# Kernel optimization log

Hardware: AMD Instinct MI355X
Metric: run time of the kernel (lower is better)

The kernel has to match this reference:

```python
import jax, jax.numpy as jnp
import numpy as np

N = 32768; D = 384; P = 3; CORR_D = 2 * 49 * P * P  # 882
G_KK = 4096; G_JK = 512
EPS = 1e-3  # LayerNorm eps in the torch module

FLOAT_NAMES = ("net","inp","corr","corr_w1","corr_b1","corr_w2","corr_b2","corr_ln_g","corr_ln_b","corr_w3","corr_b3","norm_g","norm_b","c1_w1","c1_b1","c1_w2","c1_b2","c2_w1","c2_b1","c2_w2","c2_b2","kk_fw","kk_fb","kk_gw","kk_gb","kk_hw","kk_hb","ij_fw","ij_fb","ij_gw","ij_gb","ij_hw","ij_hb","g_ln1_g","g_ln1_b","g1_gw","g1_gb","g1_r1w","g1_r1b","g1_r2w","g1_r2b","g_ln2_g","g_ln2_b","g2_gw","g2_gb","g2_r1w","g2_r1b","g2_r2w","g2_r2b","d_w","d_b","w_w","w_b")

def _ln(x, g, b):
    m = jnp.mean(x, -1, keepdims=True)
    v = jnp.mean((x - m) ** 2, -1, keepdims=True)
    return (x - m) * jax.lax.rsqrt(v + EPS) * g + b

def _mlp2(x, w1, b1, w2, b2):
    return jax.nn.relu(x @ w1 + b1) @ w2 + b2

def _gated_residual(x, gw, gb, r1w, r1b, r2w, r2b):
    gate = jax.nn.sigmoid(x @ gw + gb)
    res = jax.nn.relu(x @ r1w + r1b) @ r2w + r2b
    return x + gate * res

def _soft_agg(x, jx, fw, fb, gw, gb, hw, hb, num_groups):
    # x: [N, D]; jx: [N] group ids -> group-wise softmax weighted sum
    logits = x @ gw + gb
    feats = x @ fw + fb
    gmax = jax.ops.segment_max(logits, jx, num_segments=num_groups)
    e = jnp.exp(logits - gmax[jx])
    den = jax.ops.segment_sum(e, jx, num_segments=num_groups)
    w = e / (den[jx] + 1e-12)
    y = jax.ops.segment_sum(feats * w, jx, num_segments=num_groups)
    return (y @ hw + hb)[jx]

def _forward(p, nix, njx, ukk, ujk):
    # corr encoder MLP
    h = jax.nn.relu(p["corr"] @ p["corr_w1"] + p["corr_b1"]) @ p["corr_w2"] + p["corr_b2"]
    h = jax.nn.relu(_ln(h, p["corr_ln_g"], p["corr_ln_b"])) @ p["corr_w3"] + p["corr_b3"]
    net = p["net"] + p["inp"] + h
    net = _ln(net, p["norm_g"], p["norm_b"])
    mask_ix = (nix >= 0).astype(net.dtype).reshape(1, -1, 1)
    mask_jx = (njx >= 0).astype(net.dtype).reshape(1, -1, 1)
    net = net + _mlp2(mask_ix * net[:, nix], p["c1_w1"], p["c1_b1"], p["c1_w2"], p["c1_b2"])
    net = net + _mlp2(mask_jx * net[:, njx], p["c2_w1"], p["c2_b1"], p["c2_w2"], p["c2_b2"])
    net = net + _soft_agg(net[0], ukk, p["kk_fw"], p["kk_fb"], p["kk_gw"], p["kk_gb"], p["kk_hw"], p["kk_hb"], G_KK)[None]
    net = net + _soft_agg(net[0], ujk, p["ij_fw"], p["ij_fb"], p["ij_gw"], p["ij_gb"], p["ij_hw"], p["ij_hb"], G_JK)[None]
    net = _ln(net, p["g_ln1_g"], p["g_ln1_b"])
    net = _gated_residual(net, p["g1_gw"], p["g1_gb"], p["g1_r1w"], p["g1_r1b"], p["g1_r2w"], p["g1_r2b"])
    net = _ln(net, p["g_ln2_g"], p["g_ln2_b"])
    net = _gated_residual(net, p["g2_gw"], p["g2_gb"], p["g2_r1w"], p["g2_r1b"], p["g2_r2w"], p["g2_r2b"])
    r = jax.nn.relu(net)
    d = r @ p["d_w"] + p["d_b"]               # GradClip is identity in forward
    w = jax.nn.sigmoid(r @ p["w_w"] + p["w_b"])
    return net, d, w

def setup_inputs() -> dict:
    key = jax.random.key(0)
    it = iter(jax.random.split(key, 64))
    def pr(*shape):
        return jax.random.normal(next(it), shape, dtype=jnp.float32) * 0.02
    z = lambda *s: jnp.zeros(s, jnp.float32)
    o = lambda *s: jnp.ones(s, jnp.float32)
    inp = {
        "net": jax.random.normal(next(it), (1, N, D), dtype=jnp.float32),
        "inp": jax.random.normal(next(it), (1, N, D), dtype=jnp.float32),
        "corr": jax.random.normal(next(it), (1, N, CORR_D), dtype=jnp.float32),
        "nix": jax.random.randint(next(it), (N,), 0, N),
        "njx": jax.random.randint(next(it), (N,), 0, N),
        "ukk": jax.random.randint(next(it), (N,), 0, G_KK),
        "ujk": jax.random.randint(next(it), (N,), 0, G_JK),
        "corr_w1": pr(CORR_D, D), "corr_b1": z(D), "corr_w2": pr(D, D), "corr_b2": z(D),
        "corr_ln_g": o(D), "corr_ln_b": z(D), "corr_w3": pr(D, D), "corr_b3": z(D),
        "norm_g": o(D), "norm_b": z(D),
        "c1_w1": pr(D, D), "c1_b1": z(D), "c1_w2": pr(D, D), "c1_b2": z(D),
        "c2_w1": pr(D, D), "c2_b1": z(D), "c2_w2": pr(D, D), "c2_b2": z(D),
        "kk_fw": pr(D, D), "kk_fb": z(D), "kk_gw": pr(D, D), "kk_gb": z(D), "kk_hw": pr(D, D), "kk_hb": z(D),
        "ij_fw": pr(D, D), "ij_fb": z(D), "ij_gw": pr(D, D), "ij_gb": z(D), "ij_hw": pr(D, D), "ij_hb": z(D),
        "g_ln1_g": o(D), "g_ln1_b": z(D),
        "g1_gw": pr(D, D), "g1_gb": z(D), "g1_r1w": pr(D, D), "g1_r1b": z(D), "g1_r2w": pr(D, D), "g1_r2b": z(D),
        "g_ln2_g": o(D), "g_ln2_b": z(D),
        "g2_gw": pr(D, D), "g2_gb": z(D), "g2_r1w": pr(D, D), "g2_r1b": z(D), "g2_r2w": pr(D, D), "g2_r2b": z(D),
        "d_w": pr(D, 2), "d_b": z(2), "w_w": pr(D, 2), "w_b": z(2),
    }
    return inp

def reference(net, inp, corr, corr_w1, corr_b1, corr_w2, corr_b2, corr_ln_g, corr_ln_b, corr_w3, corr_b3, norm_g, norm_b, c1_w1, c1_b1, c1_w2, c1_b2, c2_w1, c2_b1, c2_w2, c2_b2, kk_fw, kk_fb, kk_gw, kk_gb, kk_hw, kk_hb, ij_fw, ij_fb, ij_gw, ij_gb, ij_hw, ij_hb, g_ln1_g, g_ln1_b, g1_gw, g1_gb, g1_r1w, g1_r1b, g1_r2w, g1_r2b, g_ln2_g, g_ln2_b, g2_gw, g2_gb, g2_r1w, g2_r1b, g2_r2w, g2_r2b, d_w, d_b, w_w, w_b, nix, njx, ukk, ujk):
    loc = locals()
    fl = {k: loc[k] for k in FLOAT_NAMES}
    return _forward(fl, nix, njx, ukk, ujk)
```

## Files before the change

kernel.cpp:

```cpp
#include <hip/hip_runtime.h>
#include <hip/hip_bf16.h>
#include <math.h>

#define NR 32768
#define DD 384
#define CDM 882
#define CDMP 896

typedef float f4 __attribute__((ext_vector_type(4)));
typedef float f32x4 __attribute__((ext_vector_type(4)));
typedef __bf16 bf16x8 __attribute__((ext_vector_type(8)));
typedef __bf16 bf16x4 __attribute__((ext_vector_type(4)));

__device__ inline f4 ld4(const float* p) { f4 v; __builtin_memcpy(&v, p, 16); return v; }
__device__ inline void st4(float* p, f4 v) { __builtin_memcpy(p, &v, 16); }
__device__ inline bf16x8 ld8h(const __bf16* p) { bf16x8 v; __builtin_memcpy(&v, p, 16); return v; }
__device__ inline void st8h(__bf16* p, bf16x8 v) { __builtin_memcpy(p, &v, 16); }

__device__ inline void gl_lds16(const void* g, void* l) {
  __builtin_amdgcn_global_load_lds(
      (const __attribute__((address_space(1))) void*)g,
      (__attribute__((address_space(3))) void*)l, 16, 0, 0);
}

__device__ inline float gred16(float v) {
#pragma unroll
  for (int o = 1; o < 16; o <<= 1) v += __shfl_xor(v, o, 64);
  return v;
}

__global__ __launch_bounds__(256) void corr2bf16_k(const float* __restrict__ src,
                                                   __bf16* __restrict__ dst) {
  int i = blockIdx.x * 256 + threadIdx.x;
  int row = i / 112, c8 = (i - row * 112) * 8;
  const float* sp = src + (size_t)row * CDM + c8;
  bf16x8 h;
  if (c8 + 8 <= CDM) {
#pragma unroll
    for (int e = 0; e < 8; ++e) h[e] = (__bf16)sp[e];
  } else {
#pragma unroll
    for (int e = 0; e < 8; ++e) h[e] = (c8 + e < CDM) ? (__bf16)sp[e] : (__bf16)0.f;
  }
  st8h(dst + (size_t)row * CDMP + c8, h);
}

struct WPtrs { const float* w[18]; };

__global__ __launch_bounds__(256) void trans_all_k(WPtrs P, __bf16* __restrict__ dst) {
  int wi = blockIdx.y;
  const float* W = P.w[wi];
  __bf16* WT = dst + (size_t)wi * DD * DD;
  int i = blockIdx.x * 256 + threadIdx.x;
  if (i >= DD * DD) return;
  int n = i / DD, k = i - n * DD;
  WT[i] = (__bf16)W[(size_t)k * DD + n];
}

__global__ __launch_bounds__(256) void trans_corr_k(const float* __restrict__ W,
                                                    __bf16* __restrict__ WT) {
  int i = blockIdx.x * 256 + threadIdx.x;
  if (i >= DD * CDMP) return;
  int n = i / CDMP, k = i - n * CDMP;
  WT[i] = (k < CDM) ? (__bf16)W[(size_t)k * DD + n] : (__bf16)0.f;
}

struct GP {
  const void* A; const __bf16* WT; const float* bias; __bf16* OUT;
  const __bf16* XRES; const __bf16* GIN;
  const float* p0; const float* p1; const float* p2; const float* p3;
  float* fout; const float* net32; const float* inp32;
  const int* idx; const __bf16* zpage; int M; int K;
};

template <int EPI, int AFP32>
__global__ __launch_bounds__(512, 1) void gemm_k(GP gp) {
  __shared__ __align__(16) __bf16 sm[2 * 32768];
  const int t = threadIdx.x;
  const int w = t >> 6, lane = t & 63;
  const int m0 = blockIdx.x * 128;
  const int fr = lane & 15, fq = lane >> 4;
  const int wr = (w >> 2) * 64, wc = (w & 3) * 96;
  const int K = gp.K;

  const __bf16* aptr[2];
  int aadv[2];
  const __bf16* bptr[6];
#pragma unroll
  for (int j = 0; j < 2; ++j) {
    int rloc = w * 16 + j * 8 + (lane >> 3);
    int cch = (lane & 7) ^ (rloc & 7);
    if constexpr (!AFP32) {
      int ar = gp.idx ? gp.idx[m0 + rloc] : (m0 + rloc);
      if (ar >= 0) { aptr[j] = (const __bf16*)gp.A + (size_t)ar * K + cch * 8; aadv[j] = 64; }
      else { aptr[j] = gp.zpage; aadv[j] = 0; }
    }
  }
#pragma unroll
  for (int j = 0; j < 6; ++j) {
    int rloc = w * 48 + j * 8 + (lane >> 3);
    int cch = (lane & 7) ^ (rloc & 7);
    bptr[j] = gp.WT + (size_t)rloc * K + cch * 8;
  }
  const float* Af = (const float*)gp.A;
  const int NT = K >> 6;

  f32x4 acc[4][6];
#pragma unroll
  for (int a = 0; a < 4; ++a)
#pragma unroll
    for (int b = 0; b < 6; ++b)
#pragma unroll
      for (int j = 0; j < 4; ++j) acc[a][b][j] = 0.f;

  auto stageG = [&](int buf) {
    __bf16* As = sm + buf * 32768;
    __bf16* Bs = As + 8192;
#pragma unroll
    for (int j = 0; j < 2; ++j) {
      gl_lds16(aptr[j], &As[(w * 16 + j * 8) * 64]);
      aptr[j] += aadv[j];
    }
#pragma unroll
    for (int j = 0; j < 6; ++j) {
      gl_lds16(bptr[j], &Bs[(w * 48 + j * 8) * 64]);
      bptr[j] += 64;
    }
  };

  auto stageF = [&](int k0) {
    __bf16* As = sm;
    __bf16* Bs = sm + 8192;
#pragma unroll
    for (int j = 0; j < 2; ++j) {
      int rr = (t >> 3) + 64 * j;
      int cc = t & 7;
      const float* ap = Af + (size_t)(m0 + rr) * K + k0 + cc * 8;
      f4 v0 = ld4(ap), v1 = ld4(ap + 4);
      bf16x8 h;
#pragma unroll
      for (int e = 0; e < 4; ++e) { h[e] = (__bf16)v0[e]; h[4 + e] = (__bf16)v1[e]; }
      *reinterpret_cast<bf16x8*>(&As[rr * 64 + ((cc ^ (rr & 7)) << 3)]) = h;
    }
#pragma unroll
    for (int j = 0; j < 6; ++j) {
      gl_lds16(bptr[j], &Bs[(w * 48 + j * 8) * 64]);
      bptr[j] += 64;
    }
  };

  auto compute = [&](int buf) {
    const __bf16* As = sm + buf * 32768;
    const __bf16* Bs = As + 8192;
#pragma unroll
    for (int kk2 = 0; kk2 < 2; ++kk2) {
      bf16x8 af[4];
      bf16x8 bv[6];
#pragma unroll
      for (int mi = 0; mi < 4; ++mi) {
        int rr = wr + mi * 16 + fr;
        af[mi] = *reinterpret_cast<const bf16x8*>(
            &As[rr * 64 + (((fq + kk2 * 4) ^ (rr & 7)) << 3)]);
      }
#pragma unroll
      for (int ni = 0; ni < 6; ++ni) {
        int rr = wc + ni * 16 + fr;
        bv[ni] = *reinterpret_cast<const bf16x8*>(
            &Bs[rr * 64 + (((fq + kk2 * 4) ^ (rr & 7)) << 3)]);
      }
#pragma unroll
      for (int mi = 0; mi < 4; ++mi)
#pragma unroll
        for (int ni = 0; ni < 6; ++ni)
          acc[mi][ni] = __builtin_amdgcn_mfma_f32_16x16x32_bf16(af[mi], bv[ni],
                                                                acc[mi][ni], 0, 0, 0);
    }
  };

  if constexpr (AFP32) {
    for (int tt = 0; tt < NT; ++tt) {
      if (tt) __syncthreads();
      stageF(tt << 6);
      __syncthreads();
      compute(0);
    }
  } else {
    stageG(0);
    int buf = 0;
    for (int tt = 0; tt < NT; ++tt) {
      if (tt + 1 < NT) {
        stageG(buf ^ 1);
        asm volatile("s_waitcnt vmcnt(8)" ::: "memory");
      } else {
        asm volatile("s_waitcnt vmcnt(0)" ::: "memory");
      }
      __builtin_amdgcn_s_barrier();
      __builtin_amdgcn_sched_barrier(0);
      compute(buf);
      __builtin_amdgcn_s_barrier();
      __builtin_amdgcn_sched_barrier(0);
      buf ^= 1;
    }
  }

  const int nw = w & 3;
  float bcol[6];
#pragma unroll
  for (int ni = 0; ni < 6; ++ni) bcol[ni] = gp.bias[wc + ni * 16 + fr];
#pragma unroll
  for (int mi = 0; mi < 4; ++mi)
#pragma unroll
    for (int ni = 0; ni < 6; ++ni)
#pragma unroll
      for (int j = 0; j < 4; ++j) acc[mi][ni][j] += bcol[ni];

  if constexpr (EPI <= 2) {
#pragma unroll
    for (int mi = 0; mi < 4; ++mi)
#pragma unroll
      for (int ni = 0; ni < 6; ++ni) {
        int col = wc + ni * 16 + fr;
#pragma unroll
        for (int j = 0; j < 4; ++j) {
          int row = m0 + wr + mi * 16 + fq * 4 + j;
          size_t o = (size_t)row * DD + col;
          float v = acc[mi][ni][j];
          if constexpr (EPI == 0) gp.OUT[o] = (__bf16)v;
          else if constexpr (EPI == 1) gp.OUT[o] = (__bf16)fmaxf(v, 0.f);
          else gp.OUT[o] = (__bf16)((float)gp.OUT[o] + v);
        }
      }
  } else {
    if constexpr (EPI == 5) {
#pragma unroll
      for (int mi = 0; mi < 4; ++mi)
#pragma unroll
        for (int ni = 0; ni < 6; ++ni) {
          int col = wc + ni * 16 + fr;
#pragma unroll
          for (int j = 0; j < 4; ++j) {
            int row = m0 + wr + mi * 16 + fq * 4 + j;
            size_t o = (size_t)row * DD + col;
            acc[mi][ni][j] += gp.net32[o] + gp.inp32[o];
          }
        }
    }
    if constexpr (EPI == 6 || EPI == 7) {
#pragma unroll
      for (int mi = 0; mi < 4; ++mi)
#pragma unroll
        for (int ni = 0; ni < 6; ++ni) {
          int col = wc + ni * 16 + fr;
#pragma unroll
          for (int j = 0; j < 4; ++j) {
            int row = m0 + wr + mi * 16 + fq * 4 + j;
            size_t o = (size_t)row * DD + col;
            float gl = (float)gp.GIN[o];
            float sg = 1.f / (1.f + expf(-gl));
            acc[mi][ni][j] = (float)gp.XRES[o] + sg * acc[mi][ni][j];
          }
        }
    }
    __syncthreads();
    if constexpr (EPI != 7) {
      float s1[4][4], s2[4][4];
#pragma unroll
      for (int mi = 0; mi < 4; ++mi)
#pragma unroll
        for (int j = 0; j < 4; ++j) { s1[mi][j] = 0.f; s2[mi][j] = 0.f; }
#pragma unroll
      for (int mi = 0; mi < 4; ++mi)
#pragma unroll
        for (int ni = 0; ni < 6; ++ni)
#pragma unroll
          for (int j = 0; j < 4; ++j) {
            float v = acc[mi][ni][j];
            s1[mi][j] += v;
            s2[mi][j] += v * v;
          }
#pragma unroll
      for (int o = 1; o < 16; o <<= 1)
#pragma unroll
        for (int mi = 0; mi < 4; ++mi)
#pragma unroll
          for (int j = 0; j < 4; ++j) {
            s1[mi][j] += __shfl_xor(s1[mi][j], o, 64);
            s2[mi][j] += __shfl_xor(s2[mi][j], o, 64);
          }
      float* lsum = (float*)sm;
      float* lsq = lsum + 512;
      if (fr == 0) {
#pragma unroll
        for (int mi = 0; mi < 4; ++mi)
#pragma unroll
          for (int j = 0; j < 4; ++j) {
            int rr = wr + mi * 16 + fq * 4 + j;
            lsum[rr * 4 + nw] = s1[mi][j];
            lsq[rr * 4 + nw] = s2[mi][j];
          }
      }
      __syncthreads();
      float mn[4][4], rs[4][4];
#pragma unroll
      for (int mi = 0; mi < 4; ++mi)
#pragma unroll
        for (int j = 0; j < 4; ++j) {
          int rr = wr + mi * 16 + fq * 4 + j;
          float S1 = lsum[rr * 4] + lsum[rr * 4 + 1] + lsum[rr * 4 + 2] + lsum[rr * 4 + 3];
          float S2 = lsq[rr * 4] + lsq[rr * 4 + 1] + lsq[rr * 4 + 2] + lsq[rr * 4 + 3];
          float m = S1 * (1.f / 384.f);
          float va = S2 * (1.f / 384.f) - m * m;
          mn[mi][j] = m;
          rs[mi][j] = rsqrtf(va + 1e-3f);
        }
#pragma unroll
      for (int ni = 0; ni < 6; ++ni) {
        int col = wc + ni * 16 + fr;
        float gg = gp.p0[col], bb = gp.p1[col];
#pragma unroll
        for (int mi = 0; mi < 4; ++mi)
#pragma unroll
          for (int j = 0; j < 4; ++j) {
            int row = m0 + wr + mi * 16 + fq * 4 + j;
            float y = (acc[mi][ni][j] - mn[mi][j]) * rs[mi][j] * gg + bb;
            if constexpr (EPI == 4) y = fmaxf(y, 0.f);
            gp.OUT[(size_t)row * DD + col] = (__bf16)y;
          }
      }
    } else {
      float c0[6], c1[6], c2[6], c3[6];
#pragma unroll
      for (int ni = 0; ni < 6; ++ni) {
        int col = wc + ni * 16 + fr;
        c0[ni] = gp.p0[2 * col];
        c1[ni] = gp.p0[2 * col + 1];
        c2[ni] = gp.p2[2 * col];
        c3[ni] = gp.p2[2 * col + 1];
      }
      float dt[4][4][4];
#pragma unroll
      for (int mi = 0; mi < 4; ++mi)
#pragma unroll
        for (int j = 0; j < 4; ++j)
#pragma unroll
          for (int q = 0; q < 4; ++q) dt[mi][j][q] = 0.f;
#pragma unroll
      for (int mi = 0; mi < 4; ++mi)
#pragma unroll
        for (int ni = 0; ni < 6; ++ni) {
          int col = wc + ni * 16 + fr;
#pragma unroll
          for (int j = 0; j < 4; ++j) {
            int row = m0 + wr + mi * 16 + fq * 4 + j;
            float v = acc[mi][ni][j];
            gp.fout[(size_t)row * DD + col] = v;
            float r = fmaxf(v, 0.f);
            dt[mi][j][0] += r * c0[ni];
            dt[mi][j][1] += r * c1[ni];
            dt[mi][j][2] += r * c2[ni];
            dt[mi][j][3] += r * c3[ni];
          }
        }
#pragma unroll
      for (int o = 1; o < 16; o <<= 1)
#pragma unroll
        for (int mi = 0; mi < 4; ++mi)
#pragma unroll
          for (int j = 0; j < 4; ++j)
#pragma unroll
            for (int q = 0; q < 4; ++q)
              dt[mi][j][q] += __shfl_xor(dt[mi][j][q], o, 64);
      float* lt = (float*)sm;
      if (fr == 0) {
#pragma unroll
        for (int mi = 0; mi < 4; ++mi)
#pragma unroll
          for (int j = 0; j < 4; ++j) {
            int rr = wr + mi * 16 + fq * 4 + j;
#pragma unroll
            for (int q = 0; q < 4; ++q) lt[(rr * 4 + nw) * 4 + q] = dt[mi][j][q];
          }
      }
      __syncthreads();
      if (nw == 0 && fr == 0) {
        float* fd = gp.fout + (size_t)NR * DD;
        float* fw = fd + (size_t)NR * 2;
#pragma unroll
        for (int mi = 0; mi < 4; ++mi)
#pragma unroll
          for (int j = 0; j < 4; ++j) {
            int rr = wr + mi * 16 + fq * 4 + j;
            int row = m0 + rr;
            float T[4];
#pragma unroll
            for (int q = 0; q < 4; ++q)
              T[q] = lt[(rr * 4 + 0) * 4 + q] + lt[(rr * 4 + 1) * 4 + q] +
                     lt[(rr * 4 + 2) * 4 + q] + lt[(rr * 4 + 3) * 4 + q];
            fd[2 * row] = T[0] + gp.p1[0];
            fd[2 * row + 1] = T[1] + gp.p1[1];
            fw[2 * row] = 1.f / (1.f + expf(-(T[2] + gp.p3[0])));
            fw[2 * row + 1] = 1.f / (1.f + expf(-(T[3] + gp.p3[1])));
          }
      }
    }
  }
}

__global__ __launch_bounds__(256) void ln_ag_k(const __bf16* __restrict__ X,
                                               const __bf16* __restrict__ z,
                                               const int* __restrict__ gid,
                                               const float* __restrict__ g,
                                               const float* __restrict__ b,
                                               __bf16* __restrict__ out) {
  int w = threadIdx.x >> 6, lane = threadIdx.x & 63;
  int s = lane & 15, qq = lane >> 4;
  int row = blockIdx.x * 16 + w * 4 + qq;
  int gr = gid[row];
  size_t base = (size_t)row * DD;
  size_t zbase = (size_t)gr * DD;
  float v[24];
#pragma unroll
  for (int i = 0; i < 3; ++i) {
    int col = (s + 16 * i) * 8;
    bf16x8 h = ld8h(X + base + col);
    bf16x8 zz = ld8h(z + zbase + col);
#pragma unroll
    for (int e = 0; e < 8; ++e) v[i * 8 + e] = (float)h[e] + (float)zz[e];
  }
  float sm = 0.f;
#pragma unroll
  for (int i = 0; i < 24; ++i) sm += v[i];
  sm = gred16(sm);
  float mean = sm * (1.f / 384.f);
  float qs = 0.f;
#pragma unroll
  for (int i = 0; i < 24; ++i) { float d = v[i] - mean; qs += d * d; }
  qs = gred16(qs);
  float rs = rsqrtf(qs * (1.f / 384.f) + 1e-3f);
#pragma unroll
  for (int i = 0; i < 3; ++i) {
    int col = (s + 16 * i) * 8;
    f4 g0 = ld4(g + col), g1 = ld4(g + col + 4);
    f4 b0 = ld4(b + col), b1 = ld4(b + col + 4);
    bf16x8 o;
#pragma unroll
    for (int e = 0; e < 4; ++e) {
      o[e] = (__bf16)((v[i * 8 + e] - mean) * rs * g0[e] + b0[e]);
      o[4 + e] = (__bf16)((v[i * 8 + 4 + e] - mean) * rs * g1[e] + b1[e]);
    }
    st8h(out + base + col, o);
  }
}

__global__ __launch_bounds__(256) void hist2_k(const int* __restrict__ ukk,
                                               const int* __restrict__ ujk,
                                               int* __restrict__ ckk,
                                               int* __restrict__ cij) {
  int i = blockIdx.x * 256 + threadIdx.x;
  atomicAdd(&ckk[ukk[i]], 1);
  atomicAdd(&cij[ujk[i]], 1);
}

__device__ inline void scan_body(const int* cnt, int* off, int* curb, int G, int* ls) {
  int t = threadIdx.x;
  int per = G / 256;
  int base = t * per;
  int s = 0;
  for (int i = 0; i < per; ++i) s += cnt[base + i];
  ls[t] = s;
  __syncthreads();
  for (int o = 1; o < 256; o <<= 1) {
    int v = (t >= o) ? ls[t - o] : 0;
    __syncthreads();
    ls[t] += v;
    __syncthreads();
  }
  int run = (t == 0) ? 0 : ls[t - 1];
  for (int i = 0; i < per; ++i) {
    off[base + i] = run;
    run += cnt[base + i];
    curb[base + i] = 0;
  }
  if (t == 255) off[G] = run;
}

__global__ __launch_bounds__(256) void scan2_k(const int* ckk, int* okk, int* qkk,
                                               const int* cij, int* oij, int* qij) {
  __shared__ int ls[256];
  if (blockIdx.x == 0) scan_body(ckk, okk, qkk, 4096, ls);
  else scan_body(cij, oij, qij, 512, ls);
}

__global__ __launch_bounds__(256) void scatter2_k(const int* __restrict__ ukk,
                                                  const int* __restrict__ ujk,
                                                  const int* __restrict__ okk,
                                                  int* __restrict__ qkk,
                                                  int* __restrict__ rkk,
                                                  const int* __restrict__ oij,
                                                  int* __restrict__ qij,
                                                  int* __restrict__ rij) {
  int i = blockIdx.x * 256 + threadIdx.x;
  int g1 = ukk[i];
  rkk[okk[g1] + atomicAdd(&qkk[g1], 1)] = i;
  int g2 = ujk[i];
  rij[oij[g2] + atomicAdd(&qij[g2], 1)] = i;
}

__global__ __launch_bounds__(384) void segagg_k(const __bf16* __restrict__ L,
                                                const __bf16* __restrict__ Ft,
                                                const int* __restrict__ rows,
                                                const int* __restrict__ off,
                                                float* __restrict__ yb) {
  int g = blockIdx.x;
  int c = threadIdx.x;
  int s = off[g], e = off[g + 1];
  float mx = -3.0e38f;
  for (int p = s; p < e; ++p) {
    int r = rows[p];
    mx = fmaxf(mx, (float)L[(size_t)r * DD + c]);
  }
  float num = 0.f, den = 0.f;
  for (int p = s; p < e; ++p) {
    int r = rows[p];
    float lv = (float)L[(size_t)r * DD + c];
    float fv = (float)Ft[(size_t)r * DD + c];
    float ev = expf(lv - mx);
    den += ev;
    num += fv * ev;
  }
  yb[(size_t)g * DD + c] = num / (den + 1e-12f);
}

__global__ __launch_bounds__(256) void addgather_k(__bf16* __restrict__ X,
                                                   const __bf16* __restrict__ z,
                                                   const int* __restrict__ gid) {
  int i = blockIdx.x * 256 + threadIdx.x;
  int row = i / 48, c = (i - row * 48) * 8;
  int g = gid[row];
  size_t lo = (size_t)row * DD + c;
  bf16x8 a = ld8h(X + lo);
  bf16x8 zz = ld8h(z + (size_t)g * DD + c);
  bf16x8 o;
#pragma unroll
  for (int e = 0; e < 8; ++e) o[e] = (__bf16)((float)a[e] + (float)zz[e]);
  st8h(X + lo, o);
}

extern "C" void kernel_launch(void* const* d_in, const int* in_sizes, int n_in,
                              void* d_out, int out_size, void* d_ws, size_t ws_size,
                              hipStream_t stream) {
  const float* in_net = (const float*)d_in[0];
  const float* in_inp = (const float*)d_in[1];
  const float* in_corr = (const float*)d_in[2];
  const int* nix = (const int*)d_in[3];
  const int* njx = (const int*)d_in[4];
  const int* ukk = (const int*)d_in[5];
  const int* ujk = (const int*)d_in[6];
  auto F = [&](int i) { return (const float*)d_in[i]; };

  constexpr size_t MiB = 1024 * 1024;
  constexpr size_t SZ_ACT = (size_t)NR * DD * 2;
  char* ws = (char*)d_ws;
  __bf16* Xc = (__bf16*)(ws);
  __bf16* T2b = (__bf16*)(ws);
  __bf16* Fb = (__bf16*)(ws + SZ_ACT);
  __bf16* zb = (__bf16*)(ws + 2 * SZ_ACT);
  float* yb = (float*)(ws + 2 * SZ_ACT + 3 * MiB);
  __bf16* T1b = (__bf16*)(ws + 60 * MiB);
  char* p = ws + 84 * MiB;
  int* rows_kk = (int*)p; p += (size_t)NR * 4;
  int* rows_ij = (int*)p; p += (size_t)NR * 4;
  int* off_kk = (int*)p; p += 8192 * 4;
  int* off_ij = (int*)p; p += 1024 * 4;
  int* cnt_kk = (int*)p; p += 4096 * 4;
  int* cnt_ij = (int*)p; p += 512 * 4;
  int* curb_kk = (int*)p; p += 4096 * 4;
  int* curb_ij = (int*)p; p += 512 * 4;
  __bf16* wt_all = (__bf16*)p; p += (size_t)18 * DD * DD * 2;
  __bf16* wt_corr1 = (__bf16*)p; p += (size_t)DD * CDMP * 2;
  __bf16* zpage = (__bf16*)p;

  const int widx[18] = {17, 19, 21, 23, 25, 27, 29, 31, 33, 35, 39, 41, 43, 47, 49, 51, 9, 13};
  WPtrs P;
  for (int i = 0; i < 18; ++i) P.w[i] = F(widx[i]);
  auto WTp = [&](int i) { return wt_all + (size_t)i * DD * DD; };

  hipMemsetAsync(zpage, 0, 256, stream);
  hipMemsetAsync(cnt_kk, 0, 4096 * 4, stream);
  hipMemsetAsync(cnt_ij, 0, 512 * 4, stream);
  trans_all_k<<<dim3(576, 18), 256, 0, stream>>>(P, wt_all);
  trans_corr_k<<<1344, 256, 0, stream>>>(F(7), wt_corr1);
  corr2bf16_k<<<NR * 112 / 256, 256, 0, stream>>>(in_corr, Xc);
  hist2_k<<<NR / 256, 256, 0, stream>>>(ukk, ujk, cnt_kk, cnt_ij);
  scan2_k<<<2, 256, 0, stream>>>(cnt_kk, off_kk, curb_kk, cnt_ij, off_ij, curb_ij);
  scatter2_k<<<NR / 256, 256, 0, stream>>>(ukk, ujk, off_kk, curb_kk, rows_kk,
                                           off_ij, curb_ij, rows_ij);

  auto G = [&](int epi, const void* A, const __bf16* WT, const float* bias,
               __bf16* OUT, const __bf16* XRES, const __bf16* GIN,
               const float* p0, const float* p1, const float* p2, const float* p3,
               float* fout, const float* n32, const float* i32,
               const int* idx, int M, int K) {
    GP gp{A, WT, bias, OUT, XRES, GIN, p0, p1, p2, p3, fout, n32, i32, idx, zpage, M, K};
    dim3 g(M / 128), b(512);
    switch (epi) {
      case 0: gemm_k<0, 0><<<g, b, 0, stream>>>(gp); break;
      case 1: gemm_k<1, 0><<<g, b, 0, stream>>>(gp); break;
      case 2: gemm_k<2, 0><<<g, b, 0, stream>>>(gp); break;
      case 4: gemm_k<4, 0><<<g, b, 0, stream>>>(gp); break;
      case 5: gemm_k<5, 0><<<g, b, 0, stream>>>(gp); break;
      case 6: gemm_k<6, 0><<<g, b, 0, stream>>>(gp); break;
      case 7: gemm_k<7, 0><<<g, b, 0, stream>>>(gp); break;
      case 8: gemm_k<0, 1><<<g, b, 0, stream>>>(gp); break;
    }
  };
  auto GS = [&](int epi, const void* A, const __bf16* WT, const float* bias,
                __bf16* OUT, const int* idx, int M, int K) {
    G(epi, A, WT, bias, OUT, nullptr, nullptr, nullptr, nullptr, nullptr, nullptr,
      nullptr, nullptr, nullptr, idx, M, K);
  };

  const int SEGB = NR * 48 / 256;

  GS(1, Xc, wt_corr1, F(8), T1b, nullptr, NR, CDMP);
  G(4, T1b, WTp(16), F(10), T2b, nullptr, nullptr, F(11), F(12), nullptr, nullptr,
    nullptr, nullptr, nullptr, nullptr, NR, DD);
  G(5, T2b, WTp(17), F(14), T1b, nullptr, nullptr, F(15), F(16), nullptr, nullptr,
    nullptr, in_net, in_inp, nullptr, NR, DD);
  GS(1, T1b, WTp(0), F(18), T2b, nix, NR, DD);
  GS(2, T2b, WTp(1), F(20), T1b, nullptr, NR, DD);
  GS(1, T1b, WTp(2), F(22), T2b, njx, NR, DD);
  GS(2, T2b, WTp(3), F(24), T1b, nullptr, NR, DD);
  GS(0, T1b, WTp(5), F(28), T2b, nullptr, NR, DD);
  GS(0, T1b, WTp(4), F(26), Fb, nullptr, NR, DD);
  segagg_k<<<4096, 384, 0, stream>>>(T2b, Fb, rows_kk, off_kk, yb);
  GS(8, yb, WTp(6), F(30), zb, nullptr, 4096, DD);
  addgather_k<<<SEGB, 256, 0, stream>>>(T1b, zb, ukk);
  GS(0, T1b, WTp(8), F(34), T2b, nullptr, NR, DD);
  GS(0, T1b, WTp(7), F(32), Fb, nullptr, NR, DD);
  segagg_k<<<512, 384, 0, stream>>>(T2b, Fb, rows_ij, off_ij, yb);
  GS(8, yb, WTp(9), F(36), zb, nullptr, 512, DD);
  ln_ag_k<<<NR / 16, 256, 0, stream>>>(T1b, zb, ujk, F(37), F(38), T2b);
  GS(0, T2b, WTp(10), F(40), Fb, nullptr, NR, DD);
  GS(1, T2b, WTp(11), F(42), T1b, nullptr, NR, DD);
  G(6, T1b, WTp(12), F(44), T2b, T2b, Fb, F(45), F(46), nullptr, nullptr,
    nullptr, nullptr, nullptr, nullptr, NR, DD);
  GS(0, T2b, WTp(13), F(48), Fb, nullptr, NR, DD);
  GS(1, T2b, WTp(14), F(50), T1b, nullptr, NR, DD);
  G(7, T1b, WTp(15), F(52), nullptr, T2b, Fb, F(53), F(54), F(55), F(56),
    (float*)d_out, nullptr, nullptr, nullptr, NR, DD);
}
```

Baseline: 608.0 us.

## Merge paired same-input GEMMs into one dual-role launch with XCD swizzle

Adds gemm2_k, which runs two GEMMs that share the same A operand in a single launch. Workgroups alternate between the two weight matrices and epilogues, and four pairs of back-to-back GEMM launches are replaced this way. It also remaps block indices so neighbouring row tiles land on the same XCD, and raises MFMA issue priority with s_setprio. The fused kernel is single-buffered with a smaller LDS footprint to allow two blocks per CU, trading the double-buffered pipeline for more occupancy and fewer launches.

```diff
diff --git a/kernel.cpp b/kernel.cpp
--- a/kernel.cpp
+++ b/kernel.cpp
@@ -27,6 +27,11 @@
 #pragma unroll
   for (int o = 1; o < 16; o <<= 1) v += __shfl_xor(v, o, 64);
   return v;
+}
+
+__device__ inline int xcd_swz(int orig, int nwg) {
+  int q = nwg >> 3, r = nwg & 7, xcd = orig & 7, lid = orig >> 3;
+  return (xcd < r ? xcd * (q + 1) : r * (q + 1) + (xcd - r) * q) + lid;
 }
 
 __global__ __launch_bounds__(256) void corr2bf16_k(const float* __restrict__ src,
@@ -73,12 +78,250 @@
   const int* idx; const __bf16* zpage; int M; int K;
 };
 
+template <int EPI>
+__device__ __forceinline__ void epilogue(const GP& gp, f32x4 (&acc)[4][6],
+                                         __bf16* sm, int m0, int w, int lane) {
+  const int fr = lane & 15, fq = lane >> 4;
+  const int wr = (w >> 2) * 64, wc = (w & 3) * 96;
+  const int nw = w & 3;
+  float bcol[6];
+#pragma unroll
+  for (int ni = 0; ni < 6; ++ni) bcol[ni] = gp.bias[wc + ni * 16 + fr];
+#pragma unroll
+  for (int mi = 0; mi < 4; ++mi)
+#pragma unroll
+    for (int ni = 0; ni < 6; ++ni)
+#pragma unroll
+      for (int j = 0; j < 4; ++j) acc[mi][ni][j] += bcol[ni];
+
+  if constexpr (EPI <= 2) {
+#pragma unroll
+    for (int mi = 0; mi < 4; ++mi)
+#pragma unroll
+      for (int ni = 0; ni < 6; ++ni) {
+        int col = wc + ni * 16 + fr;
+#pragma unroll
+        for (int j = 0; j < 4; ++j) {
+          int row = m0 + wr + mi * 16 + fq * 4 + j;
+          size_t o = (size_t)row * DD + col;
+          float v = acc[mi][ni][j];
+          if constexpr (EPI == 0) gp.OUT[o] = (__bf16)v;
+          else if constexpr (EPI == 1) gp.OUT[o] = (__bf16)fmaxf(v, 0.f);
+          else gp.OUT[o] = (__bf16)((float)gp.OUT[o] + v);
+        }
+      }
+  } else {
+    if constexpr (EPI == 5) {
+#pragma unroll
+      for (int mi = 0; mi < 4; ++mi)
+#pragma unroll
+        for (int ni = 0; ni < 6; ++ni) {
+          int col = wc + ni * 16 + fr;
+#pragma unroll
+          for (int j = 0; j < 4; ++j) {
+            int row = m0 + wr + mi * 16 + fq * 4 + j;
+            size_t o = (size_t)row * DD + col;
+            acc[mi][ni][j] += gp.net32[o] + gp.inp32[o];
+          }
+        }
+    }
+    if constexpr (EPI == 6 || EPI == 7) {
+#pragma unroll
+      for (int mi = 0; mi < 4; ++mi)
+#pragma unroll
+        for (int ni = 0; ni < 6; ++ni) {
+          int col = wc + ni * 16 + fr;
+#pragma unroll
+          for (int j = 0; j < 4; ++j) {
+            int row = m0 + wr + mi * 16 + fq * 4 + j;
+            size_t o = (size_t)row * DD + col;
+            float gl = (float)gp.GIN[o];
+            float sg = 1.f / (1.f + expf(-gl));
+            acc[mi][ni][j] = (float)gp.XRES[o] + sg * acc[mi][ni][j];
+          }
+        }
+    }
+    __syncthreads();
+    if constexpr (EPI != 7) {
+      float s1[4][4], s2[4][4];
+#pragma unroll
+      for (int mi = 0; mi < 4; ++mi)
+#pragma unroll
+        for (int j = 0; j < 4; ++j) { s1[mi][j] = 0.f; s2[mi][j] = 0.f; }
+#pragma unroll
+      for (int mi = 0; mi < 4; ++mi)
+#pragma unroll
+        for (int ni = 0; ni < 6; ++ni)
+#pragma unroll
+          for (int j = 0; j < 4; ++j) {
+            float v = acc[mi][ni][j];
+            s1[mi][j] += v;
+            s2[mi][j] += v * v;
+          }
+#pragma unroll
+      for (int o = 1; o < 16; o <<= 1)
+#pragma unroll
+        for (int mi = 0; mi < 4; ++mi)
+#pragma unroll
+          for (int j = 0; j < 4; ++j) {
+            s1[mi][j] += __shfl_xor(s1[mi][j], o, 64);
+            s2[mi][j] += __shfl_xor(s2[mi][j], o, 64);
+          }
+      float* lsum = (float*)sm;
+      float* lsq = lsum + 512;
+      if (fr == 0) {
+#pragma unroll
+        for (int mi = 0; mi < 4; ++mi)
+#pragma unroll
+          for (int j = 0; j < 4; ++j) {
+            int rr = wr + mi * 16 + fq * 4 + j;
+            lsum[rr * 4 + nw] = s1[mi][j];
+            lsq[rr * 4 + nw] = s2[mi][j];
+          }
+      }
+      __syncthreads();
+      float mn[4][4], rs[4][4];
+#pragma unroll
+      for (int mi = 0; mi < 4; ++mi)
+#pragma unroll
+        for (int j = 0; j < 4; ++j) {
+          int rr = wr + mi * 16 + fq * 4 + j;
+          float S1 = lsum[rr * 4] + lsum[rr * 4 + 1] + lsum[rr * 4 + 2] + lsum[rr * 4 + 3];
+          float S2 = lsq[rr * 4] + lsq[rr * 4 + 1] + lsq[rr * 4 + 2] + lsq[rr * 4 + 3];
+          float m = S1 * (1.f / 384.f);
+          float va = S2 * (1.f / 384.f) - m * m;
+          mn[mi][j] = m;
+          rs[mi][j] = rsqrtf(va + 1e-3f);
+        }
+#pragma unroll
+      for (int ni = 0; ni < 6; ++ni) {
+        int col = wc + ni * 16 + fr;
+        float gg = gp.p0[col], bb = gp.p1[col];
+#pragma unroll
+        for (int mi = 0; mi < 4; ++mi)
+#pragma unroll
+          for (int j = 0; j < 4; ++j) {
+            int row = m0 + wr + mi * 16 + fq * 4 + j;
+            float y = (acc[mi][ni][j] - mn[mi][j]) * rs[mi][j] * gg + bb;
+            if constexpr (EPI == 4) y = fmaxf(y, 0.f);
+            gp.OUT[(size_t)row * DD + col] = (__bf16)y;
+          }
+      }
+    } else {
+      float c0[6], c1[6], c2[6], c3[6];
+#pragma unroll
+      for (int ni = 0; ni < 6; ++ni) {
+        int col = wc + ni * 16 + fr;
+        c0[ni] = gp.p0[2 * col];
+        c1[ni] = gp.p0[2 * col + 1];
+        c2[ni] = gp.p2[2 * col];
+        c3[ni] = gp.p2[2 * col + 1];
+      }
+      float dt[4][4][4];
+#pragma unroll
+      for (int mi = 0; mi < 4; ++mi)
+#pragma unroll
+        for (int j = 0; j < 4; ++j)
+#pragma unroll
+          for (int q = 0; q < 4; ++q) dt[mi][j][q] = 0.f;
+#pragma unroll
+      for (int mi = 0; mi < 4; ++mi)
+#pragma unroll
+        for (int ni = 0; ni < 6; ++ni) {
+          int col = wc + ni * 16 + fr;
+#pragma unroll
+          for (int j = 0; j < 4; ++j) {
+            int row = m0 + wr + mi * 16 + fq * 4 + j;
+            float v = acc[mi][ni][j];
+            gp.fout[(size_t)row * DD + col] = v;
+            float r = fmaxf(v, 0.f);
+            dt[mi][j][0] += r * c0[ni];
+            dt[mi][j][1] += r * c1[ni];
+            dt[mi][j][2] += r * c2[ni];
+            dt[mi][j][3] += r * c3[ni];
+          }
+        }
+#pragma unroll
+      for (int o = 1; o < 16; o <<= 1)
+#pragma unroll
+        for (int mi = 0; mi < 4; ++mi)
+#pragma unroll
+          for (int j = 0; j < 4; ++j)
+#pragma unroll
+            for (int q = 0; q < 4; ++q)
+              dt[mi][j][q] += __shfl_xor(dt[mi][j][q], o, 64);
+      float* lt = (float*)sm;
+      if (fr == 0) {
+#pragma unroll
+        for (int mi = 0; mi < 4; ++mi)
+#pragma unroll
+          for (int j = 0; j < 4; ++j) {
+            int rr = wr + mi * 16 + fq * 4 + j;
+#pragma unroll
+            for (int q = 0; q < 4; ++q) lt[(rr * 4 + nw) * 4 + q] = dt[mi][j][q];
+          }
+      }
+      __syncthreads();
+      if (nw == 0 && fr == 0) {
+        float* fd = gp.fout + (size_t)NR * DD;
+        float* fw = fd + (size_t)NR * 2;
+#pragma unroll
+        for (int mi = 0; mi < 4; ++mi)
+#pragma unroll
+          for (int j = 0; j < 4; ++j) {
+            int rr = wr + mi * 16 + fq * 4 + j;
+            int row = m0 + rr;
+            float T[4];
+#pragma unroll
+            for (int q = 0; q < 4; ++q)
+              T[q] = lt[(rr * 4 + 0) * 4 + q] + lt[(rr * 4 + 1) * 4 + q] +
+                     lt[(rr * 4 + 2) * 4 + q] + lt[(rr * 4 + 3) * 4 + q];
+            fd[2 * row] = T[0] + gp.p1[0];
+            fd[2 * row + 1] = T[1] + gp.p1[1];
+            fw[2 * row] = 1.f / (1.f + expf(-(T[2] + gp.p3[0])));
+            fw[2 * row + 1] = 1.f / (1.f + expf(-(T[3] + gp.p3[1])));
+          }
+      }
+    }
+  }
+}
+
+__device__ __forceinline__ void mfma_block(const __bf16* As, const __bf16* Bs,
+                                           f32x4 (&acc)[4][6], int wr, int wc,
+                                           int fr, int fq) {
+#pragma unroll
+  for (int kk2 = 0; kk2 < 2; ++kk2) {
+    bf16x8 af[4];
+    bf16x8 bv[6];
+#pragma unroll
+    for (int mi = 0; mi < 4; ++mi) {
+      int rr = wr + mi * 16 + fr;
+      af[mi] = *reinterpret_cast<const bf16x8*>(
+          &As[rr * 64 + (((fq + kk2 * 4) ^ (rr & 7)) << 3)]);
+    }
+#pragma unroll
+    for (int ni = 0; ni < 6; ++ni) {
+      int rr = wc + ni * 16 + fr;
+      bv[ni] = *reinterpret_cast<const bf16x8*>(
+          &Bs[rr * 64 + (((fq + kk2 * 4) ^ (rr & 7)) << 3)]);
+    }
+    __builtin_amdgcn_s_setprio(1);
+#pragma unroll
+    for (int mi = 0; mi < 4; ++mi)
+#pragma unroll
+      for (int ni = 0; ni < 6; ++ni)
+        acc[mi][ni] = __builtin_amdgcn_mfma_f32_16x16x32_bf16(af[mi], bv[ni],
+                                                              acc[mi][ni], 0, 0, 0);
+    __builtin_amdgcn_s_setprio(0);
+  }
+}
+
 template <int EPI, int AFP32>
 __global__ __launch_bounds__(512, 1) void gemm_k(GP gp) {
   __shared__ __align__(16) __bf16 sm[2 * 32768];
   const int t = threadIdx.x;
   const int w = t >> 6, lane = t & 63;
-  const int m0 = blockIdx.x * 128;
+  const int m0 = xcd_swz(blockIdx.x, gridDim.x) * 128;
   const int fr = lane & 15, fq = lane >> 4;
   const int wr = (w >> 2) * 64, wc = (w & 3) * 96;
   const int K = gp.K;
@@ -149,40 +392,12 @@
     }
   };
 
-  auto compute = [&](int buf) {
-    const __bf16* As = sm + buf * 32768;
-    const __bf16* Bs = As + 8192;
-#pragma unroll
-    for (int kk2 = 0; kk2 < 2; ++kk2) {
-      bf16x8 af[4];
-      bf16x8 bv[6];
-#pragma unroll
-      for (int mi = 0; mi < 4; ++mi) {
-        int rr = wr + mi * 16 + fr;
-        af[mi] = *reinterpret_cast<const bf16x8*>(
-            &As[rr * 64 + (((fq + kk2 * 4) ^ (rr & 7)) << 3)]);
-      }
-#pragma unroll
-      for (int ni = 0; ni < 6; ++ni) {
-        int rr = wc + ni * 16 + fr;
-        bv[ni] = *reinterpret_cast<const bf16x8*>(
-            &Bs[rr * 64 + (((fq + kk2 * 4) ^ (rr & 7)) << 3)]);
-      }
-#pragma unroll
-      for (int mi = 0; mi < 4; ++mi)
-#pragma unroll
-        for (int ni = 0; ni < 6; ++ni)
-          acc[mi][ni] = __builtin_amdgcn_mfma_f32_16x16x32_bf16(af[mi], bv[ni],
-                                                                acc[mi][ni], 0, 0, 0);
-    }
-  };
-
   if constexpr (AFP32) {
     for (int tt = 0; tt < NT; ++tt) {
       if (tt) __syncthreads();
       stageF(tt << 6);
       __syncthreads();
-      compute(0);
+      mfma_block(sm, sm + 8192, acc, wr, wc, fr, fq);
     }
   } else {
     stageG(0);
@@ -196,214 +411,69 @@
       }
       __builtin_amdgcn_s_barrier();
       __builtin_amdgcn_sched_barrier(0);
-      compute(buf);
+      mfma_block(sm + buf * 32768, sm + buf * 32768 + 8192, acc, wr, wc, fr, fq);
       __builtin_amdgcn_s_barrier();
       __builtin_amdgcn_sched_barrier(0);
       buf ^= 1;
     }
   }
-
-  const int nw = w & 3;
-  float bcol[6];
-#pragma unroll
-  for (int ni = 0; ni < 6; ++ni) bcol[ni] = gp.bias[wc + ni * 16 + fr];
-#pragma unroll
-  for (int mi = 0; mi < 4; ++mi)
-#pragma unroll
-    for (int ni = 0; ni < 6; ++ni)
-#pragma unroll
-      for (int j = 0; j < 4; ++j) acc[mi][ni][j] += bcol[ni];
-
-  if constexpr (EPI <= 2) {
-#pragma unroll
-    for (int mi = 0; mi < 4; ++mi)
-#pragma unroll
-      for (int ni = 0; ni < 6; ++ni) {
-        int col = wc + ni * 16 + fr;
-#pragma unroll
-        for (int j = 0; j < 4; ++j) {
-          int row = m0 + wr + mi * 16 + fq * 4 + j;
-          size_t o = (size_t)row * DD + col;
-          float v = acc[mi][ni][j];
-          if constexpr (EPI == 0) gp.OUT[o] = (__bf16)v;
-          else if constexpr (EPI == 1) gp.OUT[o] = (__bf16)fmaxf(v, 0.f);
-          else gp.OUT[o] = (__bf16)((float)gp.OUT[o] + v);
-        }
-      }
-  } else {
-    if constexpr (EPI == 5) {
-#pragma unroll
-      for (int mi = 0; mi < 4; ++mi)
-#pragma unroll
-        for (int ni = 0; ni < 6; ++ni) {
-          int col = wc + ni * 16 + fr;
-#pragma unroll
-          for (int j = 0; j < 4; ++j) {
-            int row = m0 + wr + mi * 16 + fq * 4 + j;
-            size_t o = (size_t)row * DD + col;
-            acc[mi][ni][j] += gp.net32[o] + gp.inp32[o];
-          }
-        }
-    }
-    if constexpr (EPI == 6 || EPI == 7) {
-#pragma unroll
-      for (int mi = 0; mi < 4; ++mi)
-#pragma unroll
-        for (int ni = 0; ni < 6; ++ni) {
-          int col = wc + ni * 16 + fr;
-#pragma unroll
-          for (int j = 0; j < 4; ++j) {
-            int row = m0 + wr + mi * 16 + fq * 4 + j;
-            size_t o = (size_t)row * DD + col;
-            float gl = (float)gp.GIN[o];
-            float sg = 1.f / (1.f + expf(-gl));
-            acc[mi][ni][j] = (float)gp.XRES[o] + sg * acc[mi][ni][j];
-          }
-        }
+  epilogue<EPI>(gp, acc, sm, m0, w, lane);
+}
+
+template <int EPIA, int EPIB>
+__global__ __launch_bounds__(512, 2) void gemm2_k(GP ga, GP gb) {
+  __shared__ __align__(16) __bf16 sm[32768];
+  const int t = threadIdx.x;
+  const int w = t >> 6, lane = t & 63;
+  int wg = xcd_swz(blockIdx.x, gridDim.x);
+  const int role = wg & 1;
+  const int m0 = (wg >> 1) * 128;
+  const GP& gp = role ? gb : ga;
+  const int fr = lane & 15, fq = lane >> 4;
+  const int wr = (w >> 2) * 64, wc = (w & 3) * 96;
+  const int K = gp.K;
+
+  const __bf16* aptr[2];
+  const __bf16* bptr[6];
+#pragma unroll
+  for (int j = 0; j < 2; ++j) {
+    int rloc = w * 16 + j * 8 + (lane >> 3);
+    int cch = (lane & 7) ^ (rloc & 7);
+    aptr[j] = (const __bf16*)gp.A + (size_t)(m0 + rloc) * K + cch * 8;
+  }
+#pragma unroll
+  for (int j = 0; j < 6; ++j) {
+    int rloc = w * 48 + j * 8 + (lane >> 3);
+    int cch = (lane & 7) ^ (rloc & 7);
+    bptr[j] = gp.WT + (size_t)rloc * K + cch * 8;
+  }
+  const int NT = K >> 6;
+
+  f32x4 acc[4][6];
+#pragma unroll
+  for (int a = 0; a < 4; ++a)
+#pragma unroll
+    for (int b = 0; b < 6; ++b)
+#pragma unroll
+      for (int j = 0; j < 4; ++j) acc[a][b][j] = 0.f;
+
+  for (int tt = 0; tt < NT; ++tt) {
+    if (tt) __syncthreads();
+#pragma unroll
+    for (int j = 0; j < 2; ++j) {
+      gl_lds16(aptr[j], &sm[(w * 16 + j * 8) * 64]);
+      aptr[j] += 64;
+    }
+#pragma unroll
+    for (int j = 0; j < 6; ++j) {
+      gl_lds16(bptr[j], &sm[8192 + (w * 48 + j * 8) * 64]);
+      bptr[j] += 64;
     }
     __syncthreads();
-    if constexpr (EPI != 7) {
-      float s1[4][4], s2[4][4];
-#pragma unroll
-      for (int mi = 0; mi < 4; ++mi)
-#pragma unroll
-        for (int j = 0; j < 4; ++j) { s1[mi][j] = 0.f; s2[mi][j] = 0.f; }
-#pragma unroll
-      for (int mi = 0; mi < 4; ++mi)
-#pragma unroll
-        for (int ni = 0; ni < 6; ++ni)
-#pragma unroll
-          for (int j = 0; j < 4; ++j) {
-            float v = acc[mi][ni][j];
-            s1[mi][j] += v;
-            s2[mi][j] += v * v;
-          }
-#pragma unroll
-      for (int o = 1; o < 16; o <<= 1)
-#pragma unroll
-        for (int mi = 0; mi < 4; ++mi)
-#pragma unroll
-          for (int j = 0; j < 4; ++j) {
-            s1[mi][j] += __shfl_xor(s1[mi][j], o, 64);
-            s2[mi][j] += __shfl_xor(s2[mi][j], o, 64);
-          }
-      float* lsum = (float*)sm;
-      float* lsq = lsum + 512;
-      if (fr == 0) {
-#pragma unroll
-        for (int mi = 0; mi < 4; ++mi)
-#pragma unroll
-          for (int j = 0; j < 4; ++j) {
-            int rr = wr + mi * 16 + fq * 4 + j;
-            lsum[rr * 4 + nw] = s1[mi][j];
-            lsq[rr * 4 + nw] = s2[mi][j];
-          }
-      }
-      __syncthreads();
-      float mn[4][4], rs[4][4];
-#pragma unroll
-      for (int mi = 0; mi < 4; ++mi)
-#pragma unroll
-        for (int j = 0; j < 4; ++j) {
-          int rr = wr + mi * 16 + fq * 4 + j;
-          float S1 = lsum[rr * 4] + lsum[rr * 4 + 1] + lsum[rr * 4 + 2] + lsum[rr * 4 + 3];
-          float S2 = lsq[rr * 4] + lsq[rr * 4 + 1] + lsq[rr * 4 + 2] + lsq[rr * 4 + 3];
-          float m = S1 * (1.f / 384.f);
-          float va = S2 * (1.f / 384.f) - m * m;
-          mn[mi][j] = m;
-          rs[mi][j] = rsqrtf(va + 1e-3f);
-        }
-#pragma unroll
-      for (int ni = 0; ni < 6; ++ni) {
-        int col = wc + ni * 16 + fr;
-        float gg = gp.p0[col], bb = gp.p1[col];
-#pragma unroll
-        for (int mi = 0; mi < 4; ++mi)
-#pragma unroll
-          for (int j = 0; j < 4; ++j) {
-            int row = m0 + wr + mi * 16 + fq * 4 + j;
-            float y = (acc[mi][ni][j] - mn[mi][j]) * rs[mi][j] * gg + bb;
-            if constexpr (EPI == 4) y = fmaxf(y, 0.f);
-            gp.OUT[(size_t)row * DD + col] = (__bf16)y;
-          }
-      }
-    } else {
-      float c0[6], c1[6], c2[6], c3[6];
-#pragma unroll
-      for (int ni = 0; ni < 6; ++ni) {
-        int col = wc + ni * 16 + fr;
-        c0[ni] = gp.p0[2 * col];
-        c1[ni] = gp.p0[2 * col + 1];
-        c2[ni] = gp.p2[2 * col];
-        c3[ni] = gp.p2[2 * col + 1];
-      }
-      float dt[4][4][4];
-#pragma unroll
-      for (int mi = 0; mi < 4; ++mi)
-#pragma unroll
-        for (int j = 0; j < 4; ++j)
-#pragma unroll
-          for (int q = 0; q < 4; ++q) dt[mi][j][q] = 0.f;
-#pragma unroll
-      for (int mi = 0; mi < 4; ++mi)
-#pragma unroll
-        for (int ni = 0; ni < 6; ++ni) {
-          int col = wc + ni * 16 + fr;
-#pragma unroll
-          for (int j = 0; j < 4; ++j) {
-            int row = m0 + wr + mi * 16 + fq * 4 + j;
-            float v = acc[mi][ni][j];
-            gp.fout[(size_t)row * DD + col] = v;
-            float r = fmaxf(v, 0.f);
-            dt[mi][j][0] += r * c0[ni];
-            dt[mi][j][1] += r * c1[ni];
-            dt[mi][j][2] += r * c2[ni];
-            dt[mi][j][3] += r * c3[ni];
-          }
-        }
-#pragma unroll
-      for (int o = 1; o < 16; o <<= 1)
-#pragma unroll
-        for (int mi = 0; mi < 4; ++mi)
-#pragma unroll
-          for (int j = 0; j < 4; ++j)
-#pragma unroll
-            for (int q = 0; q < 4; ++q)
-              dt[mi][j][q] += __shfl_xor(dt[mi][j][q], o, 64);
-      float* lt = (float*)sm;
-      if (fr == 0) {
-#pragma unroll
-        for (int mi = 0; mi < 4; ++mi)
-#pragma unroll
-          for (int j = 0; j < 4; ++j) {
-            int rr = wr + mi * 16 + fq * 4 + j;
-#pragma unroll
-            for (int q = 0; q < 4; ++q) lt[(rr * 4 + nw) * 4 + q] = dt[mi][j][q];
-          }
-      }
-      __syncthreads();
-      if (nw == 0 && fr == 0) {
-        float* fd = gp.fout + (size_t)NR * DD;
-        float* fw = fd + (size_t)NR * 2;
-#pragma unroll
-        for (int mi = 0; mi < 4; ++mi)
-#pragma unroll
-          for (int j = 0; j < 4; ++j) {
-            int rr = wr + mi * 16 + fq * 4 + j;
-            int row = m0 + rr;
-            float T[4];
-#pragma unroll
-            for (int q = 0; q < 4; ++q)
-              T[q] = lt[(rr * 4 + 0) * 4 + q] + lt[(rr * 4 + 1) * 4 + q] +
-                     lt[(rr * 4 + 2) * 4 + q] + lt[(rr * 4 + 3) * 4 + q];
-            fd[2 * row] = T[0] + gp.p1[0];
-            fd[2 * row + 1] = T[1] + gp.p1[1];
-            fw[2 * row] = 1.f / (1.f + expf(-(T[2] + gp.p3[0])));
-            fw[2 * row + 1] = 1.f / (1.f + expf(-(T[3] + gp.p3[1])));
-          }
-      }
-    }
-  }
+    mfma_block(sm, sm + 8192, acc, wr, wc, fr, fq);
+  }
+  if (role == 0) epilogue<EPIA>(gp, acc, sm, m0, w, lane);
+  else epilogue<EPIB>(gp, acc, sm, m0, w, lane);
 }
 
 __global__ __launch_bounds__(256) void ln_ag_k(const __bf16* __restrict__ X,
@@ -596,15 +666,21 @@
   scatter2_k<<<NR / 256, 256, 0, stream>>>(ukk, ujk, off_kk, curb_kk, rows_kk,
                                            off_ij, curb_ij, rows_ij);
 
+  auto mkGP = [&](const void* A, const __bf16* WT, const float* bias, __bf16* OUT,
+                  const __bf16* XRES, const __bf16* GIN, const float* p0,
+                  const float* p1, const float* p2, const float* p3, float* fout,
+                  const float* n32, const float* i32, const int* idx, int M, int K) {
+    return GP{A, WT, bias, OUT, XRES, GIN, p0, p1, p2, p3, fout, n32, i32, idx, zpage, M, K};
+  };
+
   auto G = [&](int epi, const void* A, const __bf16* WT, const float* bias,
                __bf16* OUT, const __bf16* XRES, const __bf16* GIN,
                const float* p0, const float* p1, const float* p2, const float* p3,
                float* fout, const float* n32, const float* i32,
                const int* idx, int M, int K) {
-    GP gp{A, WT, bias, OUT, XRES, GIN, p0, p1, p2, p3, fout, n32, i32, idx, zpage, M, K};
+    GP gp = mkGP(A, WT, bias, OUT, XRES, GIN, p0, p1, p2, p3, fout, n32, i32, idx, M, K);
     dim3 g(M / 128), b(512);
     switch (epi) {
-      case 0: gemm_k<0, 0><<<g, b, 0, stream>>>(gp); break;
       case 1: gemm_k<1, 0><<<g, b, 0, stream>>>(gp); break;
       case 2: gemm_k<2, 0><<<g, b, 0, stream>>>(gp); break;
       case 4: gemm_k<4, 0><<<g, b, 0, stream>>>(gp); break;
@@ -614,39 +690,47 @@
       case 8: gemm_k<0, 1><<<g, b, 0, stream>>>(gp); break;
     }
   };
-  auto GS = [&](int epi, const void* A, const __bf16* WT, const float* bias,
-                __bf16* OUT, const int* idx, int M, int K) {
-    G(epi, A, WT, bias, OUT, nullptr, nullptr, nullptr, nullptr, nullptr, nullptr,
-      nullptr, nullptr, nullptr, idx, M, K);
+  auto G2 = [&](const void* A, const __bf16* WTa, const float* ba, __bf16* Oa,
+                const __bf16* WTb, const float* bb, __bf16* Ob, int epib, int M) {
+    GP ga = mkGP(A, WTa, ba, Oa, nullptr, nullptr, nullptr, nullptr, nullptr,
+                 nullptr, nullptr, nullptr, nullptr, nullptr, M, DD);
+    GP gb = mkGP(A, WTb, bb, Ob, nullptr, nullptr, nullptr, nullptr, nullptr,
+                 nullptr, nullptr, nullptr, nullptr, nullptr, M, DD);
+    dim3 g(2 * (M / 128)), b(512);
+    if (epib == 0) gemm2_k<0, 0><<<g, b, 0, stream>>>(ga, gb);
+    else gemm2_k<0, 1><<<g, b, 0, stream>>>(ga, gb);
   };
 
   const int SEGB = NR * 48 / 256;
 
-  GS(1, Xc, wt_corr1, F(8), T1b, nullptr, NR, CDMP);
+  G(1, Xc, wt_corr1, F(8), T1b, nullptr, nullptr, nullptr, nullptr, nullptr,
+    nullptr, nullptr, nullptr, nullptr, nullptr, NR, CDMP);
   G(4, T1b, WTp(16), F(10), T2b, nullptr, nullptr, F(11), F(12), nullptr, nullptr,
     nullptr, nullptr, nullptr, nullptr, NR, DD);
   G(5, T2b, WTp(17), F(14), T1b, nullptr, nullptr, F(15), F(16), nullptr, nullptr,
     nullptr, in_net, in_inp, nullptr, NR, DD);
-  GS(1, T1b, WTp(0), F(18), T2b, nix, NR, DD);
-  GS(2, T2b, WTp(1), F(20), T1b, nullptr, NR, DD);
-  GS(1, T1b, WTp(2), F(22), T2b, njx, NR, DD);
-  GS(2, T2b, WTp(3), F(24), T1b, nullptr, NR, DD);
-  GS(0, T1b, WTp(5), F(28), T2b, nullptr, NR, DD);
-  GS(0, T1b, WTp(4), F(26), Fb, nullptr, NR, DD);
+  G(1, T1b, WTp(0), F(18), T2b, nullptr, nullptr, nullptr, nullptr, nullptr,
+    nullptr, nullptr, nullptr, nullptr, nix, NR, DD);
+  G(2, T2b, WTp(1), F(20), T1b, nullptr, nullptr, nullptr, nullptr, nullptr,
+    nullptr, nullptr, nullptr, nullptr, nullptr, NR, DD);
+  G(1, T1b, WTp(2), F(22), T2b, nullptr, nullptr, nullptr, nullptr, nullptr,
+    nullptr, nullptr, nullptr, nullptr, njx, NR, DD);
+  G(2, T2b, WTp(3), F(24), T1b, nullptr, nullptr, nullptr, nullptr, nullptr,
+    nullptr, nullptr, nullptr, nullptr, nullptr, NR, DD);
+  G2(T1b, WTp(5), F(28), T2b, WTp(4), F(26), Fb, 0, NR);
   segagg_k<<<4096, 384, 0, stream>>>(T2b, Fb, rows_kk, off_kk, yb);
-  GS(8, yb, WTp(6), F(30), zb, nullptr, 4096, DD);
+  G(8, yb, WTp(6), F(30), zb, nullptr, nullptr, nullptr, nullptr, nullptr,
+    nullptr, nullptr, nullptr, nullptr, nullptr, 4096, DD);
   addgather_k<<<SEGB, 256, 0, stream>>>(T1b, zb, ukk);
-  GS(0, T1b, WTp(8), F(34), T2b, nullptr, NR, DD);
-  GS(0, T1b, WTp(7), F(32), Fb, nullptr, NR, DD);
+  G2(T1b, WTp(8), F(34), T2b, WTp(7), F(32), Fb, 0, NR);
   segagg_k<<<512, 384, 0, stream>>>(T2b, Fb, rows_ij, off_ij, yb);
-  GS(8, yb, WTp(9), F(36), zb, nullptr, 512, DD);
+  G(8, yb, WTp(9), F(36), zb, nullptr, nullptr, nullptr, nullptr, nullptr,
+    nullptr, nullptr, nullptr, nullptr, nullptr, 512, DD);
   ln_ag_k<<<NR / 16, 256, 0, stream>>>(T1b, zb, ujk, F(37), F(38), T2b);
-  GS(0, T2b, WTp(10), F(40), Fb, nullptr, NR, DD);
-  GS(1, T2b, WTp(11), F(42), T1b, nullptr, NR, DD);
+  G2(T2b, WTp(10), F(40), Fb, WTp(11), F(42), T1b, 1, NR);
   G(6, T1b, WTp(12), F(44), T2b, T2b, Fb, F(45), F(46), nullptr, nullptr,
     nullptr, nullptr, nullptr, nullptr, NR, DD);
-  GS(0, T2b, WTp(13), F(48), Fb, nullptr, NR, DD);
-  GS(1, T2b, WTp(14), F(50), T1b, nullptr, NR, DD);
+  G2(T2b, WTp(13), F(48), Fb, WTp(14), F(50), T1b, 1, NR);
   G(7, T1b, WTp(15), F(52), nullptr, T2b, Fb, F(53), F(54), F(55), F(56),
     (float*)d_out, nullptr, nullptr, nullptr, NR, DD);
 }
```

Result: slower. 634.6 us (+4.4%).
